# Performance work log

Measured on AMD Instinct MI355X. Metric: run time of the kernel, lower is better.

The kernel has to match this reference:

```python
import jax, jax.numpy as jnp
import numpy as np
from jax import lax

A = 3          # anchors per scale
C = 80         # num foreground classes (COCO)
NMS_THRESH = 0.45
NMS_TOPK = 400
POST_NMS = 100


def setup_inputs() -> dict:
    key = jax.random.key(0)
    k0, k1, k2 = jax.random.split(key, 3)
    B = 8
    ch = A * (C + 5)  # 255
    # raw head outputs (pre-decode conv activations), modest scale so exp() stays sane
    tip0 = jax.random.normal(k0, (B, ch, 19, 19), jnp.float32) * 0.5
    tip1 = jax.random.normal(k1, (B, ch, 38, 38), jnp.float32) * 0.5
    tip2 = jax.random.normal(k2, (B, ch, 76, 76), jnp.float32) * 0.5
    # standard YOLOv3 COCO anchors, deepest scale (stride 32) first
    anchors0 = jnp.array([[116., 90.], [156., 198.], [373., 326.]], jnp.float32)
    anchors1 = jnp.array([[30., 61.], [62., 45.], [59., 119.]], jnp.float32)
    anchors2 = jnp.array([[10., 13.], [16., 30.], [33., 23.]], jnp.float32)
    return dict(tip0=tip0, tip1=tip1, tip2=tip2,
                anchors0=anchors0, anchors1=anchors1, anchors2=anchors2)


def _decode(tip, anchors, stride):
    """YOLOOutputV3 inference decode. tip: (B, A*(C+5), H, W)."""
    B, _, H, W = tip.shape
    # (B, A*(C+5), H*W) -> (B, H*W, A, C+5)
    pred = tip.reshape(B, A * (C + 5), H * W).transpose(0, 2, 1).reshape(B, H * W, A, C + 5)
    gx, gy = jnp.meshgrid(jnp.arange(W), jnp.arange(H))       # each (H, W)
    offsets = jnp.stack([gx, gy], -1).reshape(1, H * W, 1, 2).astype(tip.dtype)
    centers = (jax.nn.sigmoid(pred[..., :2]) + offsets) * stride          # (B,HW,A,2)
    scales = jnp.exp(pred[..., 2:4]) * anchors.reshape(1, 1, A, 2)        # (B,HW,A,2)
    conf = jax.nn.sigmoid(pred[..., 4:5])                                 # objectness
    cls_scores = jax.nn.sigmoid(pred[..., 5:]) * conf                      # (B,HW,A,C)
    wh = scales * 0.5
    bbox = jnp.concatenate([centers - wh, centers + wh], -1)               # corner format
    return bbox.reshape(B, H * W * A, 4), cls_scores.reshape(B, H * W * A, C)


def _pairwise_iou(b):
    """b: (K,4) corner boxes -> (K,K) IoU."""
    x1, y1, x2, y2 = b[:, 0], b[:, 1], b[:, 2], b[:, 3]
    area = jnp.maximum(x2 - x1, 0.) * jnp.maximum(y2 - y1, 0.)
    iw = jnp.maximum(jnp.minimum(x2[:, None], x2[None, :]) - jnp.maximum(x1[:, None], x1[None, :]), 0.)
    ih = jnp.maximum(jnp.minimum(y2[:, None], y2[None, :]) - jnp.maximum(y1[:, None], y1[None, :]), 0.)
    inter = iw * ih
    return inter / (area[:, None] + area[None, :] - inter + 1e-12)


def _nms_single(det):
    """Class-aware greedy NMS on one image. det: (M,6) = (cid, score, x1,y1,x2,y2)."""
    K = NMS_TOPK
    _, idx = lax.top_k(det[:, 1], K)     # sort by score, keep top K
    d = det[idx]                          # (K,6), descending score
    iou = _pairwise_iou(d[:, 2:6])
    same = d[:, 0][:, None] == d[:, 0][None, :]   # only same class suppresses
    valid = d[:, 1] > 0.
    rng = jnp.arange(K)

    def body(i, keep):
        sup = (iou[i] > NMS_THRESH) & same[i] & (rng > i) & keep[i] & valid[i]
        return keep & ~sup

    keep = lax.fori_loop(0, K, body, jnp.ones((K,), bool)) & valid
    d = jnp.where(keep[:, None], d, jnp.full_like(d, -1.))
    order = jnp.argsort(-d[:, 1])         # kept (sorted) first, suppressed (-1) last
    return d[order][:POST_NMS]            # (POST_NMS, 6)


def _detect(tip0, tip1, tip2, anchors0, anchors1, anchors2):
    dets = []
    for tip, anc, stride in ((tip0, anchors0, 32), (tip1, anchors1, 16), (tip2, anchors2, 8)):
        bbox, scores = _decode(tip, anc, stride)          # (B,N,4), (B,N,C)
        B, N, _ = bbox.shape
        ids = jnp.broadcast_to(jnp.arange(C, dtype=bbox.dtype)[None, None, :, None], (B, N, C, 1))
        sc = scores[..., None]                            # (B,N,C,1)
        bx = jnp.broadcast_to(bbox[:, :, None, :], (B, N, C, 4))
        dets.append(jnp.concatenate([ids, sc, bx], -1).reshape(B, N * C, 6))
    det = jnp.concatenate(dets, 1)                        # (B, M, 6)
    return jax.vmap(_nms_single)(det)                     # (B, POST_NMS, 6)


def reference(tip0, tip1, tip2, anchors0, anchors1, anchors2):
    res = _detect(tip0, tip1, tip2, anchors0, anchors1, anchors2)
    ids = res[..., 0:1]
    scores = res[..., 1:2]
    bboxes = res[..., 2:6]
    return ids, scores, bboxes
```

## Files before the change

kernel.cpp:

```cpp
#include <hip/hip_runtime.h>
#include <stdint.h>

#define NUMA 3
#define NUMC 80
#define CAP  49152
#define CAP2 8192
#define KTOP 400
#define POST 100
#define NBIN1 2048
#define EQCAP 1024
#define KEY0 0x3EE66666u
#define LBUF 2048
#define NMASK (KTOP * 7)

typedef float f32x4 __attribute__((ext_vector_type(4)));

__device__ __forceinline__ float sigmoidf_(float x) { return 1.0f / (1.0f + expf(-x)); }
__device__ __forceinline__ unsigned uminu(unsigned a, unsigned b) { return a < b ? a : b; }

__global__ void init_kernel(unsigned* __restrict__ p) {
    int i = blockIdx.x * blockDim.x + threadIdx.x;
    if (i < NBIN1 * 16 + 40) p[i] = 0;
}

__global__ __launch_bounds__(256) void score_main(
        const float* __restrict__ t0, const float* __restrict__ t1,
        const float* __restrict__ t2,
        unsigned* __restrict__ ccnt, unsigned* __restrict__ ckey,
        unsigned* __restrict__ cidx, unsigned* __restrict__ histN)
{
    __shared__ unsigned lkey[LBUF], lidx[LBUF];
    __shared__ unsigned lh[NBIN1];
    __shared__ unsigned lcnt, lbase;
    const int tid = threadIdx.x;
    if (tid == 0) lcnt = 0;
    for (int i = tid; i < NBIN1; i += 256) lh[i] = 0;
    __syncthreads();

    const int ba = blockIdx.z;
    const int b = ba / 3, a = ba - 3 * b;
    const int c0 = blockIdx.y * 8;
    const int cx = blockIdx.x;

    #define LEMIT(SC, IDX) do { \
        unsigned key_ = __float_as_uint(SC); \
        if (key_ >= KEY0) { \
            atomicAdd(&lh[(key_ - KEY0) >> 13], 1u); \
            unsigned pos_ = atomicAdd(&lcnt, 1u); \
            if (pos_ < LBUF) { lkey[pos_] = key_; lidx[pos_] = (IDX); } \
        } \
    } while (0)

    if (cx < 2) {
        const int hw = cx * 256 + tid;
        if (hw < 361) {
            const float* base = t0 + (size_t)(b * 255 + a * 85) * 361;
            float cr = base[4 * 361 + hw];
            const float* p0 = base + (size_t)(5 + c0) * 361 + hw;
            float x0 = p0[0 * 361], x1 = p0[1 * 361], x2 = p0[2 * 361], x3 = p0[3 * 361];
            float x4 = p0[4 * 361], x5 = p0[5 * 361], x6 = p0[6 * 361], x7 = p0[7 * 361];
            float cf = sigmoidf_(cr);
            unsigned ib = (unsigned)((hw * NUMA + a) * NUMC + c0);
            LEMIT(sigmoidf_(x0) * cf, ib + 0);
            LEMIT(sigmoidf_(x1) * cf, ib + 1);
            LEMIT(sigmoidf_(x2) * cf, ib + 2);
            LEMIT(sigmoidf_(x3) * cf, ib + 3);
            LEMIT(sigmoidf_(x4) * cf, ib + 4);
            LEMIT(sigmoidf_(x5) * cf, ib + 5);
            LEMIT(sigmoidf_(x6) * cf, ib + 6);
            LEMIT(sigmoidf_(x7) * cf, ib + 7);
        }
    } else {
        const float* tip; int vHW, v, candOff;
        if (cx < 4) { tip = t1; vHW = 361;  v = (cx - 2) * 256 + tid; candOff = 86640; }
        else        { tip = t2; vHW = 1444; v = (cx - 4) * 256 + tid; candOff = 433200; }
        if (v < vHW) {
            const f32x4* bp = (const f32x4*)(tip + (size_t)(b * 255 + a * 85) * (size_t)(vHW * 4));
            f32x4 cv = bp[(size_t)4 * vHW + v];
            const f32x4* p0 = bp + (size_t)(5 + c0) * vHW + v;
            f32x4 s0 = p0[0 * (size_t)vHW], s1 = p0[1 * (size_t)vHW];
            f32x4 s2 = p0[2 * (size_t)vHW], s3 = p0[3 * (size_t)vHW];
            f32x4 s4 = p0[4 * (size_t)vHW], s5 = p0[5 * (size_t)vHW];
            f32x4 s6 = p0[6 * (size_t)vHW], s7 = p0[7 * (size_t)vHW];
            float cf0 = sigmoidf_(cv[0]), cf1 = sigmoidf_(cv[1]);
            float cf2 = sigmoidf_(cv[2]), cf3 = sigmoidf_(cv[3]);
            unsigned ib0 = (unsigned)(candOff + (v * 4 * NUMA + a) * NUMC + c0);
            #define EMIT4(S, U) do { \
                unsigned ib = ib0 + (U); \
                LEMIT(sigmoidf_((S)[0]) * cf0, ib); \
                LEMIT(sigmoidf_((S)[1]) * cf1, ib + 240); \
                LEMIT(sigmoidf_((S)[2]) * cf2, ib + 480); \
                LEMIT(sigmoidf_((S)[3]) * cf3, ib + 720); \
            } while (0)
            EMIT4(s0, 0); EMIT4(s1, 1); EMIT4(s2, 2); EMIT4(s3, 3);
            EMIT4(s4, 4); EMIT4(s5, 5); EMIT4(s6, 6); EMIT4(s7, 7);
            #undef EMIT4
        }
    }
    #undef LEMIT

    __syncthreads();
    if (tid == 0) {
        unsigned c = lcnt;
        if (c > LBUF) {
            atomicOr(&ccnt[b], 0x80000000u);
            lbase = 0xFFFFFFFFu;
        } else {
            lbase = atomicAdd(&ccnt[b], c);
        }
    }
    __syncthreads();
    unsigned c = uminu(lcnt, (unsigned)LBUF);
    unsigned basep = lbase;
    if (basep != 0xFFFFFFFFu) {
        for (unsigned i = tid; i < c; i += 256) {
            unsigned p = basep + i;
            if (p < CAP) {
                ckey[(size_t)b * CAP + p] = lkey[i];
                cidx[(size_t)b * CAP + p] = lidx[i];
            }
        }
    }
    unsigned* gh = histN + b * NBIN1;
    for (int i = tid; i < NBIN1; i += 256) {
        unsigned v2 = lh[i];
        if (v2) atomicAdd(&gh[i], v2);
    }
}

__device__ __forceinline__ void wave_select(const unsigned* h, int nbins, unsigned rank,
                                            unsigned* resv, int tid)
{
    if (tid >= 64) return;
    const int lane = tid;
    const int cs = nbins >> 6;
    unsigned v = 0;
    for (int k = 0; k < cs; k++) {
        int off = (k + lane) & (cs - 1);
        v += h[lane * cs + off];
    }
    unsigned S = v;
    #pragma unroll
    for (int o = 1; o < 64; o <<= 1) {
        unsigned t = (unsigned)__shfl_down((int)S, o);
        if (lane + o < 64) S += t;
    }
    unsigned long long bm = __ballot(S >= rank);
    if (bm == 0ull) bm = 1ull;
    int C = 63 - __builtin_clzll(bm);
    unsigned SC = (unsigned)__builtin_amdgcn_readlane((int)S, C);
    unsigned vC = (unsigned)__builtin_amdgcn_readlane((int)v, C);
    unsigned rem = rank - (SC - vC);
    unsigned w = (lane < cs) ? h[C * cs + lane] : 0u;
    unsigned T = w;
    #pragma unroll
    for (int o = 1; o < 64; o <<= 1) {
        unsigned t = (unsigned)__shfl_down((int)T, o);
        if (lane + o < 64) T += t;
    }
    unsigned long long bm2 = __ballot((T >= rem) && (lane < cs));
    if (bm2 == 0ull) bm2 = 1ull;
    int B = 63 - __builtin_clzll(bm2);
    unsigned TB = (unsigned)__builtin_amdgcn_readlane((int)T, B);
    unsigned wB = (unsigned)__builtin_amdgcn_readlane((int)w, B);
    if (lane == 0) {
        resv[0] = (unsigned)(C * cs + B);
        resv[1] = rem - (TB - wB);
    }
}

__global__ __launch_bounds__(256) void findcut_v(const unsigned* __restrict__ histN,
                                                 unsigned* __restrict__ cutfloor,
                                                 unsigned* __restrict__ ccnt,
                                                 unsigned* __restrict__ flags) {
    __shared__ unsigned h[NBIN1];
    __shared__ unsigned resv[2];
    int b = blockIdx.x;
    for (int i = threadIdx.x; i < NBIN1; i += 256) h[i] = histN[b * NBIN1 + i];
    __syncthreads();
    wave_select(h, NBIN1, KTOP, resv, threadIdx.x);
    __syncthreads();
    if (threadIdx.x == 0) {
        unsigned c = ccnt[b];
        bool ok = (c >= KTOP) && (c <= CAP);
        flags[b] = ok ? 1u : 0u;
        if (ok) {
            cutfloor[b] = KEY0 + (resv[0] << 13);
        } else {
            cutfloor[b] = 0u;
            ccnt[b] = 0;
        }
    }
}

__global__ __launch_bounds__(256) void fb_hist(
        const float* __restrict__ t0, const float* __restrict__ t1,
        const float* __restrict__ t2,
        unsigned* __restrict__ histF, const unsigned* __restrict__ flags)
{
    const int ba = blockIdx.z;
    const int b = ba / 3, a = ba - 3 * b;
    if (flags[b]) return;
    __shared__ unsigned lh[NBIN1];
    const int tid = threadIdx.x;
    for (int i = tid; i < NBIN1; i += 256) lh[i] = 0;
    __syncthreads();
    const int c0 = blockIdx.y * 8;
    const int cx = blockIdx.x;
    if (cx < 2) {
        const int hw = cx * 256 + tid;
        if (hw < 361) {
            const float* base = t0 + (size_t)(b * 255 + a * 85) * 361;
            float cf = sigmoidf_(base[4 * 361 + hw]);
            for (int u = 0; u < 8; u++) {
                float sc = sigmoidf_(base[(size_t)(5 + c0 + u) * 361 + hw]) * cf;
                atomicAdd(&lh[__float_as_uint(sc) >> 19], 1u);
            }
        }
    } else {
        const float* tip; int vHW, v;
        if (cx < 4) { tip = t1; vHW = 361;  v = (cx - 2) * 256 + tid; }
        else        { tip = t2; vHW = 1444; v = (cx - 4) * 256 + tid; }
        if (v < vHW) {
            const f32x4* bp = (const f32x4*)(tip + (size_t)(b * 255 + a * 85) * (size_t)(vHW * 4));
            f32x4 cv = bp[(size_t)4 * vHW + v];
            float cf[4] = { sigmoidf_(cv[0]), sigmoidf_(cv[1]), sigmoidf_(cv[2]), sigmoidf_(cv[3]) };
            for (int u = 0; u < 8; u++) {
                f32x4 s = bp[(size_t)(5 + c0 + u) * vHW + v];
                for (int l = 0; l < 4; l++)
                    atomicAdd(&lh[__float_as_uint(sigmoidf_(s[l]) * cf[l]) >> 19], 1u);
            }
        }
    }
    __syncthreads();
    unsigned* gh = histF + b * NBIN1;
    for (int i = tid; i < NBIN1; i += 256) {
        unsigned v2 = lh[i];
        if (v2) atomicAdd(&gh[i], v2);
    }
}

__global__ __launch_bounds__(256) void fb_cut(const unsigned* __restrict__ histF,
                                              unsigned* __restrict__ cutb,
                                              const unsigned* __restrict__ flags) {
    int b = blockIdx.x;
    if (flags[b]) return;
    __shared__ unsigned h[NBIN1];
    __shared__ unsigned resv[2];
    for (int i = threadIdx.x; i < NBIN1; i += 256) h[i] = histF[b * NBIN1 + i];
    __syncthreads();
    wave_select(h, NBIN1, KTOP, resv, threadIdx.x);
    __syncthreads();
    if (threadIdx.x == 0) cutb[b] = resv[0];
}

__global__ __launch_bounds__(256) void fb_compact(
        const float* __restrict__ t0, const float* __restrict__ t1,
        const float* __restrict__ t2,
        const unsigned* __restrict__ cutb, unsigned* __restrict__ ccnt,
        unsigned* __restrict__ ckey, unsigned* __restrict__ cidx,
        const unsigned* __restrict__ flags)
{
    const int ba = blockIdx.z;
    const int b = ba / 3, a = ba - 3 * b;
    if (flags[b]) return;
    const int tid = threadIdx.x;
    const int c0 = blockIdx.y * 8;
    const int cx = blockIdx.x;
    unsigned cutkey = cutb[b] << 19;

    if (cx < 2) {
        const int hw = cx * 256 + tid;
        if (hw < 361) {
            const float* base = t0 + (size_t)(b * 255 + a * 85) * 361;
            float cf = sigmoidf_(base[4 * 361 + hw]);
            for (int u = 0; u < 8; u++) {
                float sc = sigmoidf_(base[(size_t)(5 + c0 + u) * 361 + hw]) * cf;
                unsigned key = __float_as_uint(sc);
                if (key >= cutkey) {
                    unsigned pos = atomicAdd(&ccnt[b], 1u);
                    if (pos < CAP) {
                        ckey[(size_t)b * CAP + pos] = key;
                        cidx[(size_t)b * CAP + pos] = (unsigned)((hw * NUMA + a) * NUMC + c0 + u);
                    }
                }
            }
        }
    } else {
        const float* tip; int vHW, v, candOff;
        if (cx < 4) { tip = t1; vHW = 361;  v = (cx - 2) * 256 + tid; candOff = 86640; }
        else        { tip = t2; vHW = 1444; v = (cx - 4) * 256 + tid; candOff = 433200; }
        if (v < vHW) {
            const f32x4* bp = (const f32x4*)(tip + (size_t)(b * 255 + a * 85) * (size_t)(vHW * 4));
            f32x4 cv = bp[(size_t)4 * vHW + v];
            float cf[4] = { sigmoidf_(cv[0]), sigmoidf_(cv[1]), sigmoidf_(cv[2]), sigmoidf_(cv[3]) };
            unsigned ib0 = (unsigned)(candOff + (v * 4 * NUMA + a) * NUMC + c0);
            for (int u = 0; u < 8; u++) {
                f32x4 s = bp[(size_t)(5 + c0 + u) * vHW + v];
                for (int l = 0; l < 4; l++) {
                    float sc = sigmoidf_(s[l]) * cf[l];
                    unsigned key = __float_as_uint(sc);
                    if (key >= cutkey) {
                        unsigned pos = atomicAdd(&ccnt[b], 1u);
                        if (pos < CAP) {
                            ckey[(size_t)b * CAP + pos] = key;
                            cidx[(size_t)b * CAP + pos] = ib0 + (unsigned)u + (unsigned)l * 240;
                        }
                    }
                }
            }
        }
    }
}

__global__ __launch_bounds__(256) void prefilter(
        const unsigned* __restrict__ ckey, const unsigned* __restrict__ cidx,
        const unsigned* __restrict__ ccnt, const unsigned* __restrict__ cutfloor,
        unsigned* __restrict__ cnt2, unsigned* __restrict__ ckey2,
        unsigned* __restrict__ cidx2)
{
    __shared__ unsigned lk[LBUF], li[LBUF];
    __shared__ unsigned lcnt, lbase;
    const int tid = threadIdx.x;
    const int b = blockIdx.z;
    if (tid == 0) lcnt = 0;
    __syncthreads();
    const unsigned n = uminu(ccnt[b], (unsigned)CAP);
    const unsigned cutf = cutfloor[b];
    const unsigned* ck = ckey + (size_t)b * CAP;
    const unsigned* ci = cidx + (size_t)b * CAP;
    for (unsigned i = blockIdx.x * 256 + tid; i < n; i += 32 * 256) {
        unsigned k = ck[i];
        if (k >= cutf) {
            unsigned p = atomicAdd(&lcnt, 1u);
            if (p < LBUF) { lk[p] = k; li[p] = ci[i]; }
        }
    }
    __syncthreads();
    if (tid == 0) lbase = atomicAdd(&cnt2[b], uminu(lcnt, (unsigned)LBUF));
    __syncthreads();
    unsigned c = uminu(lcnt, (unsigned)LBUF);
    for (unsigned i = tid; i < c; i += 256) {
        unsigned p = lbase + i;
        if (p < CAP2) {
            ckey2[(size_t)b * CAP2 + p] = lk[i];
            cidx2[(size_t)b * CAP2 + p] = li[i];
        }
    }
}

__global__ __launch_bounds__(512) void topk_kernel(
        const float* __restrict__ t0, const float* __restrict__ t1,
        const float* __restrict__ t2,
        const float* __restrict__ anc0, const float* __restrict__ anc1,
        const float* __restrict__ anc2,
        const unsigned* __restrict__ ckey, const unsigned* __restrict__ cidx,
        const unsigned* __restrict__ ccnt,
        const unsigned* __restrict__ ckey2, const unsigned* __restrict__ cidx2,
        const unsigned* __restrict__ cnt2,
        float* __restrict__ dX1, float* __restrict__ dY1,
        float* __restrict__ dX2, float* __restrict__ dY2,
        float* __restrict__ dSC, unsigned* __restrict__ dCID)
{
    const int b = blockIdx.x;
    const int tid = threadIdx.x;
    const int T = 512;

    __shared__ unsigned hist[4096];
    __shared__ unsigned resv[2];
    __shared__ unsigned selk[512], seli[512];
    __shared__ unsigned eqi[EQCAP];
    __shared__ unsigned cnts[2];

    unsigned n2 = cnt2[b];
    const unsigned* ck; const unsigned* ci; unsigned n;
    if (n2 <= (unsigned)CAP2) {
        ck = ckey2 + (size_t)b * CAP2; ci = cidx2 + (size_t)b * CAP2; n = n2;
    } else {
        ck = ckey + (size_t)b * CAP; ci = cidx + (size_t)b * CAP;
        n = uminu(ccnt[b], (unsigned)CAP);
    }

    for (int i = tid; i < NBIN1; i += T) hist[i] = 0;
    __syncthreads();
    for (unsigned i = tid; i < n; i += T) atomicAdd(&hist[ck[i] >> 19], 1u);
    __syncthreads();
    wave_select(hist, NBIN1, KTOP, resv, tid);
    __syncthreads();
    unsigned b1 = resv[0], r2 = resv[1];
    __syncthreads();

    for (int i = tid; i < 4096; i += T) hist[i] = 0;
    __syncthreads();
    for (unsigned i = tid; i < n; i += T) {
        unsigned k = ck[i];
        if ((k >> 19) == b1) atomicAdd(&hist[(k >> 7) & 0xFFFu], 1u);
    }
    __syncthreads();
    wave_select(hist, 4096, r2, resv, tid);
    __syncthreads();
    unsigned b2 = resv[0], r3 = resv[1];
    __syncthreads();

    for (int i = tid; i < 128; i += T) hist[i] = 0;
    __syncthreads();
    unsigned pref = (b1 << 12) | b2;
    for (unsigned i = tid; i < n; i += T) {
        unsigned k = ck[i];
        if ((k >> 7) == pref) atomicAdd(&hist[k & 127u], 1u);
    }
    __syncthreads();
    wave_select(hist, 128, r3, resv, tid);
    __syncthreads();
    unsigned b3 = resv[0], needEq = resv[1];
    unsigned K400 = (b1 << 19) | (b2 << 7) | b3;
    __syncthreads();

    selk[tid] = 0u; seli[tid] = 0xFFFFFFFFu;
    for (int i = tid; i < EQCAP; i += T) eqi[i] = 0xFFFFFFFFu;
    if (tid == 0) { cnts[0] = 0; cnts[1] = 0; }
    __syncthreads();
    for (unsigned i = tid; i < n; i += T) {
        unsigned k = ck[i];
        if (k > K400) {
            unsigned p = atomicAdd(&cnts[0], 1u);
            if (p < KTOP) { selk[p] = k; seli[p] = ci[i]; }
        } else if (k == K400) {
            unsigned q = atomicAdd(&cnts[1], 1u);
            if (q < EQCAP) eqi[q] = ci[i];
        }
    }
    __syncthreads();
    unsigned selCnt = uminu(cnts[0], (unsigned)KTOP);
    unsigned eqN   = uminu(cnts[1], (unsigned)EQCAP);

    if (eqN > needEq) {
        int P2 = 1; while ((unsigned)P2 < eqN) P2 <<= 1;
        for (int k2 = 2; k2 <= P2; k2 <<= 1) {
            for (int j = k2 >> 1; j > 0; j >>= 1) {
                __syncthreads();
                for (int i = tid; i < P2; i += T) {
                    int ixj = i ^ j;
                    if (ixj > i && ixj < P2) {
                        unsigned va = eqi[i], vb = eqi[ixj];
                        bool up = ((i & k2) == 0);
                        if (up ? (va > vb) : (va < vb)) { eqi[i] = vb; eqi[ixj] = va; }
                    }
                }
            }
        }
        __syncthreads();
    }
    for (unsigned t2v = tid; t2v < needEq; t2v += T) {
        unsigned p = selCnt + t2v;
        if (p < KTOP) { selk[p] = K400; seli[p] = eqi[t2v]; }
    }
    __syncthreads();

    for (int k2 = 2; k2 <= 512; k2 <<= 1) {
        int j = k2 >> 1;
        for (; j >= 64; j >>= 1) {
            __syncthreads();
            int i = tid, ixj = i ^ j;
            if (ixj > i) {
                unsigned ka = selk[i], kb = selk[ixj], ia = seli[i], ib = seli[ixj];
                bool before = (ka > kb) || (ka == kb && ia < ib);
                bool up = ((i & k2) == 0);
                if (up ? !before : before) {
                    selk[i] = kb; selk[ixj] = ka; seli[i] = ib; seli[ixj] = ia;
                }
            }
        }
        __syncthreads();
        for (; j > 0; j >>= 1) {
            int i = tid, ixj = i ^ j;
            if (ixj > i) {
                unsigned ka = selk[i], kb = selk[ixj], ia = seli[i], ib = seli[ixj];
                bool before = (ka > kb) || (ka == kb && ia < ib);
                bool up = ((i & k2) == 0);
                if (up ? !before : before) {
                    selk[i] = kb; selk[ixj] = ka; seli[i] = ib; seli[ixj] = ia;
                }
            }
        }
    }
    __syncthreads();

    if (tid < KTOP) {
        unsigned idx = seli[tid];
        const float* tip; const float* anc; int HW, W, candOff; float strideF;
        if (idx < 86640u)       { tip = t0; anc = anc0; HW = 361;  W = 19; strideF = 32.f; candOff = 0; }
        else if (idx < 433200u) { tip = t1; anc = anc1; HW = 1444; W = 38; strideF = 16.f; candOff = 86640; }
        else                    { tip = t2; anc = anc2; HW = 5776; W = 76; strideF = 8.f;  candOff = 433200; }
        unsigned local = idx - (unsigned)candOff;
        int cls = (int)(local % NUMC);
        int nn  = (int)(local / NUMC);
        int a = nn % NUMA, hwl = nn / NUMA;
        const float* base = tip + (size_t)(b * 255 + a * 85) * HW + hwl;
        float tx = base[0];
        float ty = base[(size_t)HW];
        float tw = base[(size_t)2 * HW];
        float th = base[(size_t)3 * HW];
        float fx = (float)(hwl % W), fy = (float)(hwl / W);
        float cx = (sigmoidf_(tx) + fx) * strideF;
        float cy = (sigmoidf_(ty) + fy) * strideF;
        float hw_ = expf(tw) * anc[2 * a]     * 0.5f;
        float hh_ = expf(th) * anc[2 * a + 1] * 0.5f;
        int o = b * KTOP + tid;
        dX1[o] = cx - hw_; dY1[o] = cy - hh_;
        dX2[o] = cx + hw_; dY2[o] = cy + hh_;
        dSC[o] = __uint_as_float(selk[tid]);
        dCID[o] = (unsigned)cls;
    }
}

__global__ __launch_bounds__(256) void mask_kernel(
        const float* __restrict__ dX1, const float* __restrict__ dY1,
        const float* __restrict__ dX2, const float* __restrict__ dY2,
        const unsigned* __restrict__ dCID, unsigned long long* __restrict__ maskG)
{
    __shared__ float lx1[KTOP], ly1[KTOP], lx2[KTOP], ly2[KTOP];
    __shared__ int lcid[KTOP];
    const int b = blockIdx.y;
    const int tid = threadIdx.x;
    for (int i = tid; i < KTOP; i += 256) {
        int o = b * KTOP + i;
        lx1[i] = dX1[o]; ly1[i] = dY1[o];
        lx2[i] = dX2[o]; ly2[i] = dY2[o];
        lcid[i] = (int)dCID[o];
    }
    __syncthreads();
    int p = blockIdx.x * 256 + tid;
    if (p < NMASK) {
        int i = p / 7, w = p - i * 7;
        float x1i = lx1[i], y1i = ly1[i], x2i = lx2[i], y2i = ly2[i];
        float ai = fmaxf(x2i - x1i, 0.f) * fmaxf(y2i - y1i, 0.f);
        int cidI = lcid[i];
        unsigned long long m = 0ull;
        int j0 = w * 64;
        int j1 = j0 + 64; if (j1 > KTOP) j1 = KTOP;
        int js = j0 > i + 1 ? j0 : i + 1;
        for (int j = js; j < j1; j++) {
            if (lcid[j] != cidI) continue;
            float iw = fminf(x2i, lx2[j]) - fmaxf(x1i, lx1[j]);
            float ih = fminf(y2i, ly2[j]) - fmaxf(y1i, ly1[j]);
            iw = fmaxf(iw, 0.f); ih = fmaxf(ih, 0.f);
            float inter = iw * ih;
            float aj = fmaxf(lx2[j] - lx1[j], 0.f) * fmaxf(ly2[j] - ly1[j], 0.f);
            float iou = inter / (ai + aj - inter + 1e-12f);
            if (iou > 0.45f) m |= (1ull << (j - j0));
        }
        maskG[(size_t)b * NMASK + p] = m;
    }
}

__global__ __launch_bounds__(512) void greedy_kernel(
        const float* __restrict__ dX1, const float* __restrict__ dY1,
        const float* __restrict__ dX2, const float* __restrict__ dY2,
        const float* __restrict__ dSC, const unsigned* __restrict__ dCID,
        const unsigned long long* __restrict__ maskG, float* __restrict__ out)
{
    __shared__ unsigned long long maskL[NMASK];
    __shared__ unsigned long long vkeep[7];
    __shared__ float oid[POST], osc[POST], obb[POST * 4];
    const int b = blockIdx.x;
    const int tid = threadIdx.x;

    for (int i = tid; i < NMASK; i += 512) maskL[i] = maskG[(size_t)b * NMASK + i];
    if (tid < POST) { oid[tid] = -1.f; osc[tid] = -1.f; }
    if (tid < POST * 4) obb[tid] = -1.f;
    __syncthreads();

    if (tid < 64) {
        const int lane = tid;
        unsigned long long keep = 0ull;
        if (lane < 7) keep = (lane == 6) ? 0xFFFFull : ~0ull;
        unsigned long long mb[8];
        #pragma unroll
        for (int k = 0; k < 8; k++)
            mb[k] = (lane < 7) ? maskL[k * 7 + lane] : 0ull;
        for (int ib = 0; ib < KTOP; ib += 8) {
            #pragma unroll
            for (int k = 0; k < 8; k++) {
                int i = ib + k;
                unsigned long long m = mb[k];
                int nf = ib + 8 + k;
                mb[k] = (lane < 7 && nf < KTOP) ? maskL[nf * 7 + lane] : 0ull;
                int w = i >> 6;
                unsigned klo = (unsigned)__builtin_amdgcn_readlane((int)(unsigned)(keep & 0xFFFFFFFFull), w);
                unsigned khi = (unsigned)__builtin_amdgcn_readlane((int)(unsigned)(keep >> 32), w);
                unsigned long long kw = ((unsigned long long)khi << 32) | klo;
                if ((kw >> (i & 63)) & 1ull) keep &= ~m;
            }
        }
        if (lane < 7) vkeep[lane] = keep;
    }
    __syncthreads();

    if (tid < KTOP) {
        int w = tid >> 6, bp = tid & 63;
        unsigned long long kw = vkeep[w];
        if ((kw >> bp) & 1ull) {
            int r = 0;
            for (int q = 0; q < w; q++) r += __popcll(vkeep[q]);
            r += __popcll(kw & ((1ull << bp) - 1ull));
            if (r < POST) {
                int o = b * KTOP + tid;
                oid[r] = (float)(int)dCID[o];
                osc[r] = dSC[o];
                obb[r * 4 + 0] = dX1[o];
                obb[r * 4 + 1] = dY1[o];
                obb[r * 4 + 2] = dX2[o];
                obb[r * 4 + 3] = dY2[o];
            }
        }
    }
    __syncthreads();
    if (tid < POST) {
        out[b * POST + tid]       = oid[tid];
        out[800 + b * POST + tid] = osc[tid];
    }
    if (tid < POST * 4) out[1600 + b * POST * 4 + tid] = obb[tid];
}

extern "C" void kernel_launch(void* const* d_in, const int* in_sizes, int n_in,
                              void* d_out, int out_size, void* d_ws, size_t ws_size,
                              hipStream_t stream)
{
    const float* tip0 = (const float*)d_in[0];
    const float* tip1 = (const float*)d_in[1];
    const float* tip2 = (const float*)d_in[2];
    const float* anc0 = (const float*)d_in[3];
    const float* anc1 = (const float*)d_in[4];
    const float* anc2 = (const float*)d_in[5];
    float* out = (float*)d_out;

    unsigned* histN    = (unsigned*)d_ws;
    unsigned* histF    = histN + 8 * NBIN1;
    unsigned* cutb     = histF + 8 * NBIN1;
    unsigned* cutfloor = cutb + 8;
    unsigned* ccnt     = cutfloor + 8;
    unsigned* cnt2     = ccnt + 8;
    unsigned* flags    = cnt2 + 8;
    unsigned* ckey     = flags + 8;
    unsigned* cidx     = ckey + (size_t)8 * CAP;
    unsigned* ckey2    = cidx + (size_t)8 * CAP;
    unsigned* cidx2    = ckey2 + (size_t)8 * CAP2;
    float*    dX1      = (float*)(cidx2 + (size_t)8 * CAP2);
    float*    dY1      = dX1 + 8 * KTOP;
    float*    dX2      = dY1 + 8 * KTOP;
    float*    dY2      = dX2 + 8 * KTOP;
    float*    dSC      = dY2 + 8 * KTOP;
    unsigned* dCID     = (unsigned*)(dSC + 8 * KTOP);
    unsigned long long* maskG = (unsigned long long*)(dCID + 8 * KTOP);

    init_kernel<<<(NBIN1 * 16 + 40 + 255) / 256, 256, 0, stream>>>(histN);

    dim3 g(10, 10, 24);
    score_main<<<g, 256, 0, stream>>>(tip0, tip1, tip2, ccnt, ckey, cidx, histN);
    findcut_v<<<8, 256, 0, stream>>>(histN, cutfloor, ccnt, flags);
    fb_hist<<<g, 256, 0, stream>>>(tip0, tip1, tip2, histF, flags);
    fb_cut<<<8, 256, 0, stream>>>(histF, cutb, flags);
    fb_compact<<<g, 256, 0, stream>>>(tip0, tip1, tip2, cutb, ccnt, ckey, cidx, flags);
    prefilter<<<dim3(32, 1, 8), 256, 0, stream>>>(ckey, cidx, ccnt, cutfloor,
                                                  cnt2, ckey2, cidx2);
    topk_kernel<<<8, 512, 0, stream>>>(tip0, tip1, tip2, anc0, anc1, anc2,
                                       ckey, cidx, ccnt, ckey2, cidx2, cnt2,
                                       dX1, dY1, dX2, dY2, dSC, dCID);
    mask_kernel<<<dim3((NMASK + 255) / 256, 8), 256, 0, stream>>>(
        dX1, dY1, dX2, dY2, dCID, maskG);
    greedy_kernel<<<8, 512, 0, stream>>>(dX1, dY1, dX2, dY2, dSC, dCID, maskG, out);
}
```

Baseline: 195.9 us.

## Fuse NMS mask into greedy kernel, fast-path small topk, shrink fallback grids

The IoU mask computation moves into the greedy NMS kernel and is built directly in shared memory. This removes one launch and the global mask round-trip, but only 8 blocks now do all the mask work. The topk kernel skips the three-pass radix select when there are at most 512 candidates and loads them straight into the sort buffer, marking empty slots so they are not decoded. The fallback histogram and compact kernels now loop over the 10 class groups inside each block, with a grid ten times smaller. This cuts launch overhead for those kernels, which usually exit early on their flags.

```diff
diff --git a/kernel.cpp b/kernel.cpp
--- a/kernel.cpp
+++ b/kernel.cpp
@@ -205,30 +205,32 @@
     const int tid = threadIdx.x;
     for (int i = tid; i < NBIN1; i += 256) lh[i] = 0;
     __syncthreads();
-    const int c0 = blockIdx.y * 8;
     const int cx = blockIdx.x;
-    if (cx < 2) {
-        const int hw = cx * 256 + tid;
-        if (hw < 361) {
-            const float* base = t0 + (size_t)(b * 255 + a * 85) * 361;
-            float cf = sigmoidf_(base[4 * 361 + hw]);
-            for (int u = 0; u < 8; u++) {
-                float sc = sigmoidf_(base[(size_t)(5 + c0 + u) * 361 + hw]) * cf;
-                atomicAdd(&lh[__float_as_uint(sc) >> 19], 1u);
-            }
-        }
-    } else {
-        const float* tip; int vHW, v;
-        if (cx < 4) { tip = t1; vHW = 361;  v = (cx - 2) * 256 + tid; }
-        else        { tip = t2; vHW = 1444; v = (cx - 4) * 256 + tid; }
-        if (v < vHW) {
-            const f32x4* bp = (const f32x4*)(tip + (size_t)(b * 255 + a * 85) * (size_t)(vHW * 4));
-            f32x4 cv = bp[(size_t)4 * vHW + v];
-            float cf[4] = { sigmoidf_(cv[0]), sigmoidf_(cv[1]), sigmoidf_(cv[2]), sigmoidf_(cv[3]) };
-            for (int u = 0; u < 8; u++) {
-                f32x4 s = bp[(size_t)(5 + c0 + u) * vHW + v];
-                for (int l = 0; l < 4; l++)
-                    atomicAdd(&lh[__float_as_uint(sigmoidf_(s[l]) * cf[l]) >> 19], 1u);
+    for (int cg = 0; cg < 10; cg++) {
+        const int c0 = cg * 8;
+        if (cx < 2) {
+            const int hw = cx * 256 + tid;
+            if (hw < 361) {
+                const float* base = t0 + (size_t)(b * 255 + a * 85) * 361;
+                float cf = sigmoidf_(base[4 * 361 + hw]);
+                for (int u = 0; u < 8; u++) {
+                    float sc = sigmoidf_(base[(size_t)(5 + c0 + u) * 361 + hw]) * cf;
+                    atomicAdd(&lh[__float_as_uint(sc) >> 19], 1u);
+                }
+            }
+        } else {
+            const float* tip; int vHW, v;
+            if (cx < 4) { tip = t1; vHW = 361;  v = (cx - 2) * 256 + tid; }
+            else        { tip = t2; vHW = 1444; v = (cx - 4) * 256 + tid; }
+            if (v < vHW) {
+                const f32x4* bp = (const f32x4*)(tip + (size_t)(b * 255 + a * 85) * (size_t)(vHW * 4));
+                f32x4 cv = bp[(size_t)4 * vHW + v];
+                float cf[4] = { sigmoidf_(cv[0]), sigmoidf_(cv[1]), sigmoidf_(cv[2]), sigmoidf_(cv[3]) };
+                for (int u = 0; u < 8; u++) {
+                    f32x4 s = bp[(size_t)(5 + c0 + u) * vHW + v];
+                    for (int l = 0; l < 4; l++)
+                        atomicAdd(&lh[__float_as_uint(sigmoidf_(s[l]) * cf[l]) >> 19], 1u);
+                }
             }
         }
     }
@@ -265,46 +267,48 @@
     const int b = ba / 3, a = ba - 3 * b;
     if (flags[b]) return;
     const int tid = threadIdx.x;
-    const int c0 = blockIdx.y * 8;
     const int cx = blockIdx.x;
     unsigned cutkey = cutb[b] << 19;
 
-    if (cx < 2) {
-        const int hw = cx * 256 + tid;
-        if (hw < 361) {
-            const float* base = t0 + (size_t)(b * 255 + a * 85) * 361;
-            float cf = sigmoidf_(base[4 * 361 + hw]);
-            for (int u = 0; u < 8; u++) {
-                float sc = sigmoidf_(base[(size_t)(5 + c0 + u) * 361 + hw]) * cf;
-                unsigned key = __float_as_uint(sc);
-                if (key >= cutkey) {
-                    unsigned pos = atomicAdd(&ccnt[b], 1u);
-                    if (pos < CAP) {
-                        ckey[(size_t)b * CAP + pos] = key;
-                        cidx[(size_t)b * CAP + pos] = (unsigned)((hw * NUMA + a) * NUMC + c0 + u);
-                    }
-                }
-            }
-        }
-    } else {
-        const float* tip; int vHW, v, candOff;
-        if (cx < 4) { tip = t1; vHW = 361;  v = (cx - 2) * 256 + tid; candOff = 86640; }
-        else        { tip = t2; vHW = 1444; v = (cx - 4) * 256 + tid; candOff = 433200; }
-        if (v < vHW) {
-            const f32x4* bp = (const f32x4*)(tip + (size_t)(b * 255 + a * 85) * (size_t)(vHW * 4));
-            f32x4 cv = bp[(size_t)4 * vHW + v];
-            float cf[4] = { sigmoidf_(cv[0]), sigmoidf_(cv[1]), sigmoidf_(cv[2]), sigmoidf_(cv[3]) };
-            unsigned ib0 = (unsigned)(candOff + (v * 4 * NUMA + a) * NUMC + c0);
-            for (int u = 0; u < 8; u++) {
-                f32x4 s = bp[(size_t)(5 + c0 + u) * vHW + v];
-                for (int l = 0; l < 4; l++) {
-                    float sc = sigmoidf_(s[l]) * cf[l];
+    for (int cg = 0; cg < 10; cg++) {
+        const int c0 = cg * 8;
+        if (cx < 2) {
+            const int hw = cx * 256 + tid;
+            if (hw < 361) {
+                const float* base = t0 + (size_t)(b * 255 + a * 85) * 361;
+                float cf = sigmoidf_(base[4 * 361 + hw]);
+                for (int u = 0; u < 8; u++) {
+                    float sc = sigmoidf_(base[(size_t)(5 + c0 + u) * 361 + hw]) * cf;
                     unsigned key = __float_as_uint(sc);
                     if (key >= cutkey) {
                         unsigned pos = atomicAdd(&ccnt[b], 1u);
                         if (pos < CAP) {
                             ckey[(size_t)b * CAP + pos] = key;
-                            cidx[(size_t)b * CAP + pos] = ib0 + (unsigned)u + (unsigned)l * 240;
+                            cidx[(size_t)b * CAP + pos] = (unsigned)((hw * NUMA + a) * NUMC + c0 + u);
+                        }
+                    }
+                }
+            }
+        } else {
+            const float* tip; int vHW, v, candOff;
+            if (cx < 4) { tip = t1; vHW = 361;  v = (cx - 2) * 256 + tid; candOff = 86640; }
+            else        { tip = t2; vHW = 1444; v = (cx - 4) * 256 + tid; candOff = 433200; }
+            if (v < vHW) {
+                const f32x4* bp = (const f32x4*)(tip + (size_t)(b * 255 + a * 85) * (size_t)(vHW * 4));
+                f32x4 cv = bp[(size_t)4 * vHW + v];
+                float cf[4] = { sigmoidf_(cv[0]), sigmoidf_(cv[1]), sigmoidf_(cv[2]), sigmoidf_(cv[3]) };
+                unsigned ib0 = (unsigned)(candOff + (v * 4 * NUMA + a) * NUMC + c0);
+                for (int u = 0; u < 8; u++) {
+                    f32x4 s = bp[(size_t)(5 + c0 + u) * vHW + v];
+                    for (int l = 0; l < 4; l++) {
+                        float sc = sigmoidf_(s[l]) * cf[l];
+                        unsigned key = __float_as_uint(sc);
+                        if (key >= cutkey) {
+                            unsigned pos = atomicAdd(&ccnt[b], 1u);
+                            if (pos < CAP) {
+                                ckey[(size_t)b * CAP + pos] = key;
+                                cidx[(size_t)b * CAP + pos] = ib0 + (unsigned)u + (unsigned)l * 240;
+                            }
                         }
                     }
                 }
@@ -381,81 +385,87 @@
         n = uminu(ccnt[b], (unsigned)CAP);
     }
 
-    for (int i = tid; i < NBIN1; i += T) hist[i] = 0;
-    __syncthreads();
-    for (unsigned i = tid; i < n; i += T) atomicAdd(&hist[ck[i] >> 19], 1u);
-    __syncthreads();
-    wave_select(hist, NBIN1, KTOP, resv, tid);
-    __syncthreads();
-    unsigned b1 = resv[0], r2 = resv[1];
-    __syncthreads();
-
-    for (int i = tid; i < 4096; i += T) hist[i] = 0;
-    __syncthreads();
-    for (unsigned i = tid; i < n; i += T) {
-        unsigned k = ck[i];
-        if ((k >> 19) == b1) atomicAdd(&hist[(k >> 7) & 0xFFFu], 1u);
-    }
-    __syncthreads();
-    wave_select(hist, 4096, r2, resv, tid);
-    __syncthreads();
-    unsigned b2 = resv[0], r3 = resv[1];
-    __syncthreads();
-
-    for (int i = tid; i < 128; i += T) hist[i] = 0;
-    __syncthreads();
-    unsigned pref = (b1 << 12) | b2;
-    for (unsigned i = tid; i < n; i += T) {
-        unsigned k = ck[i];
-        if ((k >> 7) == pref) atomicAdd(&hist[k & 127u], 1u);
-    }
-    __syncthreads();
-    wave_select(hist, 128, r3, resv, tid);
-    __syncthreads();
-    unsigned b3 = resv[0], needEq = resv[1];
-    unsigned K400 = (b1 << 19) | (b2 << 7) | b3;
-    __syncthreads();
-
-    selk[tid] = 0u; seli[tid] = 0xFFFFFFFFu;
-    for (int i = tid; i < EQCAP; i += T) eqi[i] = 0xFFFFFFFFu;
-    if (tid == 0) { cnts[0] = 0; cnts[1] = 0; }
-    __syncthreads();
-    for (unsigned i = tid; i < n; i += T) {
-        unsigned k = ck[i];
-        if (k > K400) {
-            unsigned p = atomicAdd(&cnts[0], 1u);
-            if (p < KTOP) { selk[p] = k; seli[p] = ci[i]; }
-        } else if (k == K400) {
-            unsigned q = atomicAdd(&cnts[1], 1u);
-            if (q < EQCAP) eqi[q] = ci[i];
-        }
-    }
-    __syncthreads();
-    unsigned selCnt = uminu(cnts[0], (unsigned)KTOP);
-    unsigned eqN   = uminu(cnts[1], (unsigned)EQCAP);
-
-    if (eqN > needEq) {
-        int P2 = 1; while ((unsigned)P2 < eqN) P2 <<= 1;
-        for (int k2 = 2; k2 <= P2; k2 <<= 1) {
-            for (int j = k2 >> 1; j > 0; j >>= 1) {
-                __syncthreads();
-                for (int i = tid; i < P2; i += T) {
-                    int ixj = i ^ j;
-                    if (ixj > i && ixj < P2) {
-                        unsigned va = eqi[i], vb = eqi[ixj];
-                        bool up = ((i & k2) == 0);
-                        if (up ? (va > vb) : (va < vb)) { eqi[i] = vb; eqi[ixj] = va; }
+    if (n <= 512u) {
+        selk[tid] = (tid < (int)n) ? ck[tid] : 0u;
+        seli[tid] = (tid < (int)n) ? ci[tid] : 0xFFFFFFFFu;
+        __syncthreads();
+    } else {
+        for (int i = tid; i < NBIN1; i += T) hist[i] = 0;
+        __syncthreads();
+        for (unsigned i = tid; i < n; i += T) atomicAdd(&hist[ck[i] >> 19], 1u);
+        __syncthreads();
+        wave_select(hist, NBIN1, KTOP, resv, tid);
+        __syncthreads();
+        unsigned b1 = resv[0], r2 = resv[1];
+        __syncthreads();
+
+        for (int i = tid; i < 4096; i += T) hist[i] = 0;
+        __syncthreads();
+        for (unsigned i = tid; i < n; i += T) {
+            unsigned k = ck[i];
+            if ((k >> 19) == b1) atomicAdd(&hist[(k >> 7) & 0xFFFu], 1u);
+        }
+        __syncthreads();
+        wave_select(hist, 4096, r2, resv, tid);
+        __syncthreads();
+        unsigned b2 = resv[0], r3 = resv[1];
+        __syncthreads();
+
+        for (int i = tid; i < 128; i += T) hist[i] = 0;
+        __syncthreads();
+        unsigned pref = (b1 << 12) | b2;
+        for (unsigned i = tid; i < n; i += T) {
+            unsigned k = ck[i];
+            if ((k >> 7) == pref) atomicAdd(&hist[k & 127u], 1u);
+        }
+        __syncthreads();
+        wave_select(hist, 128, r3, resv, tid);
+        __syncthreads();
+        unsigned b3 = resv[0], needEq = resv[1];
+        unsigned K400 = (b1 << 19) | (b2 << 7) | b3;
+        __syncthreads();
+
+        selk[tid] = 0u; seli[tid] = 0xFFFFFFFFu;
+        for (int i = tid; i < EQCAP; i += T) eqi[i] = 0xFFFFFFFFu;
+        if (tid == 0) { cnts[0] = 0; cnts[1] = 0; }
+        __syncthreads();
+        for (unsigned i = tid; i < n; i += T) {
+            unsigned k = ck[i];
+            if (k > K400) {
+                unsigned p = atomicAdd(&cnts[0], 1u);
+                if (p < KTOP) { selk[p] = k; seli[p] = ci[i]; }
+            } else if (k == K400) {
+                unsigned q = atomicAdd(&cnts[1], 1u);
+                if (q < EQCAP) eqi[q] = ci[i];
+            }
+        }
+        __syncthreads();
+        unsigned selCnt = uminu(cnts[0], (unsigned)KTOP);
+        unsigned eqN   = uminu(cnts[1], (unsigned)EQCAP);
+
+        if (eqN > needEq) {
+            int P2 = 1; while ((unsigned)P2 < eqN) P2 <<= 1;
+            for (int k2 = 2; k2 <= P2; k2 <<= 1) {
+                for (int j = k2 >> 1; j > 0; j >>= 1) {
+                    __syncthreads();
+                    for (int i = tid; i < P2; i += T) {
+                        int ixj = i ^ j;
+                        if (ixj > i && ixj < P2) {
+                            unsigned va = eqi[i], vb = eqi[ixj];
+                            bool up = ((i & k2) == 0);
+                            if (up ? (va > vb) : (va < vb)) { eqi[i] = vb; eqi[ixj] = va; }
+                        }
                     }
                 }
             }
-        }
-        __syncthreads();
-    }
-    for (unsigned t2v = tid; t2v < needEq; t2v += T) {
-        unsigned p = selCnt + t2v;
-        if (p < KTOP) { selk[p] = K400; seli[p] = eqi[t2v]; }
-    }
-    __syncthreads();
+            __syncthreads();
+        }
+        for (unsigned t2v = tid; t2v < needEq; t2v += T) {
+            unsigned p = selCnt + t2v;
+            if (p < KTOP) { selk[p] = K400; seli[p] = eqi[t2v]; }
+        }
+        __syncthreads();
+    }
 
     for (int k2 = 2; k2 <= 512; k2 <<= 1) {
         int j = k2 >> 1;
@@ -486,7 +496,7 @@
     }
     __syncthreads();
 
-    if (tid < KTOP) {
+    if (tid < KTOP && seli[tid] != 0xFFFFFFFFu) {
         unsigned idx = seli[tid];
         const float* tip; const float* anc; int HW, W, candOff; float strideF;
         if (idx < 86640u)       { tip = t0; anc = anc0; HW = 361;  W = 19; strideF = 32.f; candOff = 0; }
@@ -514,24 +524,31 @@
     }
 }
 
-__global__ __launch_bounds__(256) void mask_kernel(
+__global__ __launch_bounds__(512) void greedy_kernel(
         const float* __restrict__ dX1, const float* __restrict__ dY1,
         const float* __restrict__ dX2, const float* __restrict__ dY2,
-        const unsigned* __restrict__ dCID, unsigned long long* __restrict__ maskG)
-{
+        const float* __restrict__ dSC, const unsigned* __restrict__ dCID,
+        float* __restrict__ out)
+{
+    __shared__ unsigned long long maskL[NMASK];
     __shared__ float lx1[KTOP], ly1[KTOP], lx2[KTOP], ly2[KTOP];
     __shared__ int lcid[KTOP];
-    const int b = blockIdx.y;
+    __shared__ unsigned long long vkeep[7];
+    __shared__ float oid[POST], osc[POST], obb[POST * 4];
+    const int b = blockIdx.x;
     const int tid = threadIdx.x;
-    for (int i = tid; i < KTOP; i += 256) {
+
+    for (int i = tid; i < KTOP; i += 512) {
         int o = b * KTOP + i;
         lx1[i] = dX1[o]; ly1[i] = dY1[o];
         lx2[i] = dX2[o]; ly2[i] = dY2[o];
         lcid[i] = (int)dCID[o];
     }
-    __syncthreads();
-    int p = blockIdx.x * 256 + tid;
-    if (p < NMASK) {
+    if (tid < POST) { oid[tid] = -1.f; osc[tid] = -1.f; }
+    if (tid < POST * 4) obb[tid] = -1.f;
+    __syncthreads();
+
+    for (int p = tid; p < NMASK; p += 512) {
         int i = p / 7, w = p - i * 7;
         float x1i = lx1[i], y1i = ly1[i], x2i = lx2[i], y2i = ly2[i];
         float ai = fmaxf(x2i - x1i, 0.f) * fmaxf(y2i - y1i, 0.f);
@@ -550,25 +567,8 @@
             float iou = inter / (ai + aj - inter + 1e-12f);
             if (iou > 0.45f) m |= (1ull << (j - j0));
         }
-        maskG[(size_t)b * NMASK + p] = m;
-    }
-}
-
-__global__ __launch_bounds__(512) void greedy_kernel(
-        const float* __restrict__ dX1, const float* __restrict__ dY1,
-        const float* __restrict__ dX2, const float* __restrict__ dY2,
-        const float* __restrict__ dSC, const unsigned* __restrict__ dCID,
-        const unsigned long long* __restrict__ maskG, float* __restrict__ out)
-{
-    __shared__ unsigned long long maskL[NMASK];
-    __shared__ unsigned long long vkeep[7];
-    __shared__ float oid[POST], osc[POST], obb[POST * 4];
-    const int b = blockIdx.x;
-    const int tid = threadIdx.x;
-
-    for (int i = tid; i < NMASK; i += 512) maskL[i] = maskG[(size_t)b * NMASK + i];
-    if (tid < POST) { oid[tid] = -1.f; osc[tid] = -1.f; }
-    if (tid < POST * 4) obb[tid] = -1.f;
+        maskL[p] = m;
+    }
     __syncthreads();
 
     if (tid < 64) {
@@ -606,12 +606,12 @@
             r += __popcll(kw & ((1ull << bp) - 1ull));
             if (r < POST) {
                 int o = b * KTOP + tid;
-                oid[r] = (float)(int)dCID[o];
+                oid[r] = (float)lcid[tid];
                 osc[r] = dSC[o];
-                obb[r * 4 + 0] = dX1[o];
-                obb[r * 4 + 1] = dY1[o];
-                obb[r * 4 + 2] = dX2[o];
-                obb[r * 4 + 3] = dY2[o];
+                obb[r * 4 + 0] = lx1[tid];
+                obb[r * 4 + 1] = ly1[tid];
+                obb[r * 4 + 2] = lx2[tid];
+                obb[r * 4 + 3] = ly2[tid];
             }
         }
     }
@@ -652,22 +652,18 @@
     float*    dY2      = dX2 + 8 * KTOP;
     float*    dSC      = dY2 + 8 * KTOP;
     unsigned* dCID     = (unsigned*)(dSC + 8 * KTOP);
-    unsigned long long* maskG = (unsigned long long*)(dCID + 8 * KTOP);
 
     init_kernel<<<(NBIN1 * 16 + 40 + 255) / 256, 256, 0, stream>>>(histN);
 
-    dim3 g(10, 10, 24);
-    score_main<<<g, 256, 0, stream>>>(tip0, tip1, tip2, ccnt, ckey, cidx, histN);
+    score_main<<<dim3(10, 10, 24), 256, 0, stream>>>(tip0, tip1, tip2, ccnt, ckey, cidx, histN);
     findcut_v<<<8, 256, 0, stream>>>(histN, cutfloor, ccnt, flags);
-    fb_hist<<<g, 256, 0, stream>>>(tip0, tip1, tip2, histF, flags);
+    fb_hist<<<dim3(10, 1, 24), 256, 0, stream>>>(tip0, tip1, tip2, histF, flags);
     fb_cut<<<8, 256, 0, stream>>>(histF, cutb, flags);
-    fb_compact<<<g, 256, 0, stream>>>(tip0, tip1, tip2, cutb, ccnt, ckey, cidx, flags);
+    fb_compact<<<dim3(10, 1, 24), 256, 0, stream>>>(tip0, tip1, tip2, cutb, ccnt, ckey, cidx, flags);
     prefilter<<<dim3(32, 1, 8), 256, 0, stream>>>(ckey, cidx, ccnt, cutfloor,
                                                   cnt2, ckey2, cidx2);
     topk_kernel<<<8, 512, 0, stream>>>(tip0, tip1, tip2, anc0, anc1, anc2,
                                        ckey, cidx, ccnt, ckey2, cidx2, cnt2,
                                        dX1, dY1, dX2, dY2, dSC, dCID);
-    mask_kernel<<<dim3((NMASK + 255) / 256, 8), 256, 0, stream>>>(
-        dX1, dY1, dX2, dY2, dCID, maskG);
-    greedy_kernel<<<8, 512, 0, stream>>>(dX1, dY1, dX2, dY2, dSC, dCID, maskG, out);
-}
+    greedy_kernel<<<8, 512, 0, stream>>>(dX1, dY1, dX2, dY2, dSC, dCID, out);
+}
```

Result: slower. 215.2 us (+9.9%).
